# Optimization experiments

Measured on AMD Instinct MI355X. Metric: run time of the kernel, lower is better.

The kernel has to match this reference:

```python
import jax, jax.numpy as jnp
import numpy as np

V, B, T, C, H, L = 32000, 4, 1024, 1024, 16, 8
HS = C // H  # head_size = 64


def _ln(x, g, b):
    m = x.mean(-1, keepdims=True)
    v = x.var(-1, keepdims=True)
    return (x - m) / jnp.sqrt(v + 1e-5) * g + b


def setup_inputs() -> dict:
    key = jax.random.key(0)
    ks = jax.random.split(key, 24)
    s = 0.02
    inp = {
        "idx": jax.random.randint(ks[0], (B, T), 0, V, dtype=jnp.int64),
        "tok_emb": jax.random.normal(ks[1], (V, C), jnp.float32) * s,
        "pos_emb": jax.random.normal(ks[2], (T, C), jnp.float32) * s,
        "Wq": jax.random.normal(ks[3], (L, H, C, HS), jnp.float32) * s,
        "Wk": jax.random.normal(ks[4], (L, H, C, HS), jnp.float32) * s,
        "Wv": jax.random.normal(ks[5], (L, H, C, HS), jnp.float32) * s,
        "Ph_w": jax.random.normal(ks[6], (L, H, HS, C), jnp.float32) * s,
        "Ph_b": jnp.zeros((L, H, C), jnp.float32),
        "Pm_w": jax.random.normal(ks[7], (L, C, C), jnp.float32) * s,
        "Pm_b": jnp.zeros((L, C), jnp.float32),
        "ln1_g": jnp.ones((L, C), jnp.float32),
        "ln1_b": jnp.zeros((L, C), jnp.float32),
        "ln2_g": jnp.ones((L, C), jnp.float32),
        "ln2_b": jnp.zeros((L, C), jnp.float32),
        "W1": jax.random.normal(ks[8], (L, C, 4 * C), jnp.float32) * s,
        "b1": jnp.zeros((L, 4 * C), jnp.float32),
        "W2": jax.random.normal(ks[9], (L, 4 * C, C), jnp.float32) * s,
        "b2": jnp.zeros((L, C), jnp.float32),
        "lnf_g": jnp.ones((C,), jnp.float32),
        "lnf_b": jnp.zeros((C,), jnp.float32),
        "head_w": jax.random.normal(ks[10], (C, V), jnp.float32) * s,
        "head_b": jnp.zeros((V,), jnp.float32),
    }
    return inp


def reference(idx, tok_emb, pos_emb, Wq, Wk, Wv, Ph_w, Ph_b, Pm_w, Pm_b,
              ln1_g, ln1_b, ln2_g, ln2_b, W1, b1, W2, b2, lnf_g, lnf_b,
              head_w, head_b):
    Bx, Tx = idx.shape
    x = tok_emb[idx] + pos_emb[:Tx]  # [B,T,C]
    mask = jnp.tril(jnp.ones((Tx, Tx), bool))
    scale = x.shape[-1] ** -0.5  # NOTE: original scales by n_embd**-0.5, not head_size
    n_layers = Wq.shape[0]
    for l in range(n_layers):
        xn = _ln(x, ln1_g[l], ln1_b[l])
        q = jnp.einsum('btc,hcs->bhts', xn, Wq[l])
        k = jnp.einsum('btc,hcs->bhts', xn, Wk[l])
        v = jnp.einsum('btc,hcs->bhts', xn, Wv[l])
        wei = jnp.einsum('bhts,bhus->bhtu', q, k) * scale
        wei = jnp.where(mask, wei, -jnp.inf)
        wei = jax.nn.softmax(wei, axis=-1)
        o = jnp.einsum('bhtu,bhus->bhts', wei, v)  # [B,H,T,HS]
        per = jnp.einsum('bhts,hsc->bhtc', o, Ph_w[l]) + Ph_b[l][None, :, None, :]
        sa = per.sum(axis=1) @ Pm_w[l] + Pm_b[l]  # combine heads, final proj
        x = x + sa
        xn2 = _ln(x, ln2_g[l], ln2_b[l])
        h = jax.nn.gelu(xn2 @ W1[l] + b1[l], approximate=False)
        x = x + h @ W2[l] + b2[l]
    x = _ln(x, lnf_g, lnf_b)
    return x @ head_w + head_b  # logits [B,T,V]
```

## Files before the change

kernel.cpp:

```cpp
#include <hip/hip_runtime.h>
#include <hip/hip_bf16.h>
#include <math.h>

static constexpr int V = 32000, B = 4, T = 1024, C = 1024, H = 16, NL = 8, HS = 64;
static constexpr int M = B * T;

typedef __bf16 bf16x8 __attribute__((ext_vector_type(8)));
typedef __bf16 bf16x4 __attribute__((ext_vector_type(4)));
typedef float f32x4 __attribute__((ext_vector_type(4)));

#define AS1 __attribute__((address_space(1)))
#define AS3 __attribute__((address_space(3)))

__global__ void k_embed(const int* __restrict__ idx, const float* __restrict__ tok,
                        const float* __restrict__ pos, float* __restrict__ x) {
  int g = blockIdx.x * blockDim.x + threadIdx.x;
  if (g >= M * C / 4) return;
  int c4 = g & 255;
  int bt = g >> 8;
  int t = bt & (T - 1);
  int row = idx[bt];
  float4 tv = *(const float4*)(tok + (size_t)row * C + c4 * 4);
  float4 pv = *(const float4*)(pos + (size_t)t * C + c4 * 4);
  float4 o;
  o.x = tv.x + pv.x; o.y = tv.y + pv.y; o.z = tv.z + pv.z; o.w = tv.w + pv.w;
  *(float4*)(x + (size_t)bt * C + c4 * 4) = o;
}

__global__ __launch_bounds__(256) void k_ln_bf(const float* __restrict__ x, const float* __restrict__ g,
                                               const float* __restrict__ b, __hip_bfloat16* __restrict__ y) {
  int row = blockIdx.x, tid = threadIdx.x;
  float4 v = ((const float4*)(x + (size_t)row * C))[tid];
  float s = v.x + v.y + v.z + v.w;
  float ss = v.x * v.x + v.y * v.y + v.z * v.z + v.w * v.w;
  for (int off = 32; off > 0; off >>= 1) {
    s += __shfl_down(s, off);
    ss += __shfl_down(ss, off);
  }
  __shared__ float sb[4], qb[4];
  int wid = tid >> 6;
  if ((tid & 63) == 0) { sb[wid] = s; qb[wid] = ss; }
  __syncthreads();
  float st = sb[0] + sb[1] + sb[2] + sb[3];
  float qt = qb[0] + qb[1] + qb[2] + qb[3];
  float mean = st * (1.0f / C);
  float var = qt * (1.0f / C) - mean * mean;
  float rstd = rsqrtf(var + 1e-5f);
  float4 gv = ((const float4*)g)[tid];
  float4 bv = ((const float4*)b)[tid];
  union { __hip_bfloat16 h[4]; ushort4 u; } pk;
  pk.h[0] = __float2bfloat16((v.x - mean) * rstd * gv.x + bv.x);
  pk.h[1] = __float2bfloat16((v.y - mean) * rstd * gv.y + bv.y);
  pk.h[2] = __float2bfloat16((v.z - mean) * rstd * gv.z + bv.z);
  pk.h[3] = __float2bfloat16((v.w - mean) * rstd * gv.w + bv.w);
  *(ushort4*)(y + (size_t)row * C + tid * 4) = pk.u;
}

__global__ __launch_bounds__(256) void k_transp(const float* __restrict__ in, __hip_bfloat16* __restrict__ out,
                                                int K, int N) {
  __shared__ float t[64][65];
  int n0 = blockIdx.x * 64, k0 = blockIdx.y * 64;
  int tx = threadIdx.x & 15, ty = threadIdx.x >> 4;
#pragma unroll
  for (int i = 0; i < 64; i += 16) {
    float4 v = *(const float4*)(in + (size_t)(k0 + ty + i) * N + n0 + tx * 4);
    t[ty + i][tx * 4 + 0] = v.x;
    t[ty + i][tx * 4 + 1] = v.y;
    t[ty + i][tx * 4 + 2] = v.z;
    t[ty + i][tx * 4 + 3] = v.w;
  }
  __syncthreads();
#pragma unroll
  for (int i = 0; i < 64; i += 16) {
    int n = ty + i;
    union { __hip_bfloat16 h[4]; ushort4 u; } pk;
#pragma unroll
    for (int j = 0; j < 4; ++j) pk.h[j] = __float2bfloat16(t[tx * 4 + j][n]);
    *(ushort4*)(out + (size_t)(n0 + n) * K + k0 + tx * 4) = pk.u;
  }
}

__global__ void k_conv(const float* __restrict__ in, __hip_bfloat16* __restrict__ out, int n4) {
  int g = blockIdx.x * blockDim.x + threadIdx.x;
  if (g >= n4) return;
  float4 v = ((const float4*)in)[g];
  union { __hip_bfloat16 h[4]; ushort4 u; } pk;
  pk.h[0] = __float2bfloat16(v.x);
  pk.h[1] = __float2bfloat16(v.y);
  pk.h[2] = __float2bfloat16(v.z);
  pk.h[3] = __float2bfloat16(v.w);
  ((ushort4*)out)[g] = pk.u;
}

__global__ __launch_bounds__(256) void k_prep_qkv(const float* __restrict__ Wq, const float* __restrict__ Wk,
                                                  const float* __restrict__ Wv, __hip_bfloat16* __restrict__ out) {
  int z = blockIdx.y;
  int sel = z >> 4, h = z & 15;
  const float* W = sel == 0 ? Wq : (sel == 1 ? Wk : Wv);
  const float* in = W + (size_t)h * C * HS;
  __hip_bfloat16* o = out + ((size_t)sel * 1024 + h * 64) * C;
  __shared__ float t[64][65];
  int k0 = blockIdx.x * 64;
  int tx = threadIdx.x & 15, ty = threadIdx.x >> 4;
#pragma unroll
  for (int i = 0; i < 64; i += 16) {
    float4 v = *(const float4*)(in + (size_t)(k0 + ty + i) * HS + tx * 4);
    t[ty + i][tx * 4 + 0] = v.x;
    t[ty + i][tx * 4 + 1] = v.y;
    t[ty + i][tx * 4 + 2] = v.z;
    t[ty + i][tx * 4 + 3] = v.w;
  }
  __syncthreads();
#pragma unroll
  for (int i = 0; i < 64; i += 16) {
    int n = ty + i;
    union { __hip_bfloat16 h4[4]; ushort4 u; } pk;
#pragma unroll
    for (int j = 0; j < 4; ++j) pk.h4[j] = __float2bfloat16(t[tx * 4 + j][n]);
    *(ushort4*)(o + (size_t)n * C + k0 + tx * 4) = pk.u;
  }
}

__global__ void k_bsum(const float* __restrict__ phb, float* __restrict__ bs) {
  int c = blockIdx.x * blockDim.x + threadIdx.x;
  if (c < C) {
    float s = 0.0f;
    for (int h = 0; h < H; ++h) s += phb[(size_t)h * C + c];
    bs[c] = s;
  }
}

__global__ void k_biascomb(const float* __restrict__ bsum, const float* __restrict__ Pm,
                           const float* __restrict__ Pmb, float* __restrict__ bc) {
  int c = blockIdx.x * blockDim.x + threadIdx.x;
  if (c < C) {
    float s = Pmb[c];
    for (int j = 0; j < C; ++j) s += bsum[j] * Pm[(size_t)j * C + c];
    bc[c] = s;
  }
}

template <int BIAS, int GELU, int RES, int OUTBF>
__global__ __launch_bounds__(256) void k_gemm_bf(const __hip_bfloat16* __restrict__ A,
                                                 const __hip_bfloat16* __restrict__ Bt,
                                                 void* Cout, const float* __restrict__ bias,
                                                 const float* res, int N, int K) {
  __shared__ __align__(16) __hip_bfloat16 As[128 * 32];
  __shared__ __align__(16) __hip_bfloat16 Bs[128 * 32];
  int bm = blockIdx.y * 128, bn = blockIdx.x * 128;
  int tid = threadIdx.x;
  int w = tid >> 6, l = tid & 63;
  int wr = (w >> 1) * 64, wc = (w & 1) * 64;
  int lr = l >> 2;
  int lk = (l & 3) * 8;
  int fr = l & 15;
  int fk = (l >> 4) * 8;
  const __hip_bfloat16* Ag = A + (size_t)bm * K;
  const __hip_bfloat16* Bg = Bt + (size_t)bn * K;
  f32x4 acc[4][4];
#pragma unroll
  for (int m = 0; m < 4; ++m)
#pragma unroll
    for (int n = 0; n < 4; ++n) acc[m][n] = (f32x4){0.f, 0.f, 0.f, 0.f};

  for (int k0 = 0; k0 < K; k0 += 32) {
    __syncthreads();
#pragma unroll
    for (int i = 0; i < 2; ++i) {
      int seg = w * 2 + i;
      int r = seg * 16 + lr;
      __builtin_amdgcn_global_load_lds((const AS1 void*)(Ag + (size_t)r * K + k0 + lk),
                                       (AS3 void*)(As + seg * 512), 16, 0, 0);
      __builtin_amdgcn_global_load_lds((const AS1 void*)(Bg + (size_t)r * K + k0 + lk),
                                       (AS3 void*)(Bs + seg * 512), 16, 0, 0);
    }
    __syncthreads();
    bf16x8 af[4], bfr[4];
#pragma unroll
    for (int m = 0; m < 4; ++m) af[m] = *(const bf16x8*)(As + ((size_t)(wr + m * 16 + fr)) * 32 + fk);
#pragma unroll
    for (int n = 0; n < 4; ++n) bfr[n] = *(const bf16x8*)(Bs + ((size_t)(wc + n * 16 + fr)) * 32 + fk);
#pragma unroll
    for (int m = 0; m < 4; ++m)
#pragma unroll
      for (int n = 0; n < 4; ++n)
        acc[m][n] = __builtin_amdgcn_mfma_f32_16x16x32_bf16(af[m], bfr[n], acc[m][n], 0, 0, 0);
  }
  int crow0 = (l >> 4) * 4;
  int ccol = l & 15;
#pragma unroll
  for (int m = 0; m < 4; ++m) {
    int row = bm + wr + m * 16 + crow0;
#pragma unroll
    for (int n = 0; n < 4; ++n) {
      int col = bn + wc + n * 16 + ccol;
      float bv = BIAS ? bias[col] : 0.0f;
#pragma unroll
      for (int r = 0; r < 4; ++r) {
        float v = acc[m][n][r] + bv;
        if (GELU) v = 0.5f * v * (1.0f + erff(v * 0.70710678118f));
        if (RES) v += res[(size_t)(row + r) * N + col];
        if (OUTBF)
          ((__hip_bfloat16*)Cout)[(size_t)(row + r) * N + col] = __float2bfloat16(v);
        else
          ((float*)Cout)[(size_t)(row + r) * N + col] = v;
      }
    }
  }
}

template <int BIAS, int GELU, int RES, int OUTBF>
__global__ __launch_bounds__(512, 2) void k_gemm256(const __hip_bfloat16* __restrict__ Ah,
                                                    const __hip_bfloat16* __restrict__ Bth,
                                                    void* Cout, const float* __restrict__ bias,
                                                    const float* res, int N, int K) {
  __shared__ __align__(16) __bf16 As[2][256 * 64];
  __shared__ __align__(16) __bf16 Bs[2][256 * 64];
  const __bf16* A = (const __bf16*)Ah;
  const __bf16* Bt = (const __bf16*)Bth;
  const int nx = N >> 8;
  const int bid = blockIdx.x;
  const int sw = ((bid & 7) * ((int)gridDim.x >> 3)) + (bid >> 3);
  const int bn = (sw % nx) << 8;
  const int bm = (sw / nx) << 8;
  const int tid = threadIdx.x, w = tid >> 6, l = tid & 63;
  const int wm = w >> 2, wn = w & 3;
  const int fr = l & 15, fg = l >> 4;
  const int srow = w * 8 + (l >> 3);
  const int scolb = ((l & 7) << 4) ^ ((l & 8) << 3) ^ ((l & 16) << 1) ^ ((l & 32) >> 1);
  const __bf16* Ag = A + (size_t)(bm + srow) * K + (scolb >> 1);
  const __bf16* Bg = Bt + (size_t)(bn + srow) * K + (scolb >> 1);
  const int arow = wm * 128 + fr;
  const int brow = wn * 64 + fr;
  const int kswz = ((fr & 1) << 6) | ((fr & 2) << 4) | ((fr & 4) << 2);

  f32x4 acc[8][4];
#pragma unroll
  for (int m = 0; m < 8; ++m)
#pragma unroll
    for (int n = 0; n < 4; ++n) acc[m][n] = (f32x4){0.f, 0.f, 0.f, 0.f};

  auto stage = [&](int bufi, size_t kel) {
    const __bf16* ag_ = Ag + kel;
    const __bf16* bg_ = Bg + kel;
#pragma unroll
    for (int jj = 0; jj < 4; ++jj)
      __builtin_amdgcn_global_load_lds((const AS1 void*)(ag_ + (size_t)jj * 64 * K),
                                       (AS3 void*)(&As[bufi][jj * 4096 + w * 512]), 16, 0, 0);
#pragma unroll
    for (int jj = 0; jj < 4; ++jj)
      __builtin_amdgcn_global_load_lds((const AS1 void*)(bg_ + (size_t)jj * 64 * K),
                                       (AS3 void*)(&Bs[bufi][jj * 4096 + w * 512]), 16, 0, 0);
  };

  const int NT = K >> 6;
  stage(0, 0);
  asm volatile("s_waitcnt vmcnt(0)" ::: "memory");
  __builtin_amdgcn_sched_barrier(0);
  __builtin_amdgcn_s_barrier();
  __builtin_amdgcn_sched_barrier(0);

  for (int t = 0; t < NT; ++t) {
    const int cb = t & 1;
    const int nb = cb ^ 1;
    bf16x8 af[4][2], bv[4][2];

#define RD_A(MG, KS) \
  (*(const bf16x8*)(&As[cb][(arow + (MG) * 16) * 64 + ((((KS) * 64 + fg * 16) ^ kswz) >> 1)]))
#define RD_B(NG, KS) \
  (*(const bf16x8*)(&Bs[cb][(brow + (NG) * 16) * 64 + ((((KS) * 64 + fg * 16) ^ kswz) >> 1)]))
#define BAR() \
  __builtin_amdgcn_sched_barrier(0); __builtin_amdgcn_s_barrier(); __builtin_amdgcn_sched_barrier(0)

#pragma unroll
    for (int m = 0; m < 4; ++m) {
      af[m][0] = RD_A(m, 0);
      af[m][1] = RD_A(m, 1);
    }
#pragma unroll
    for (int n = 0; n < 2; ++n) {
      bv[n][0] = RD_B(n, 0);
      bv[n][1] = RD_B(n, 1);
    }
    if (t + 1 < NT) stage(nb, (size_t)(t + 1) * 64);
    BAR();
    __builtin_amdgcn_s_setprio(1);
#pragma unroll
    for (int m = 0; m < 4; ++m)
#pragma unroll
      for (int n = 0; n < 2; ++n)
#pragma unroll
        for (int ks = 0; ks < 2; ++ks)
          acc[m][n] = __builtin_amdgcn_mfma_f32_16x16x32_bf16(af[m][ks], bv[n][ks], acc[m][n], 0, 0, 0);
    __builtin_amdgcn_s_setprio(0);
    BAR();

#pragma unroll
    for (int n = 0; n < 2; ++n) {
      bv[2 + n][0] = RD_B(2 + n, 0);
      bv[2 + n][1] = RD_B(2 + n, 1);
    }
    BAR();
    __builtin_amdgcn_s_setprio(1);
#pragma unroll
    for (int m = 0; m < 4; ++m)
#pragma unroll
      for (int n = 0; n < 2; ++n)
#pragma unroll
        for (int ks = 0; ks < 2; ++ks)
          acc[m][2 + n] = __builtin_amdgcn_mfma_f32_16x16x32_bf16(af[m][ks], bv[2 + n][ks], acc[m][2 + n], 0, 0, 0);
    __builtin_amdgcn_s_setprio(0);
    BAR();

#pragma unroll
    for (int m = 0; m < 4; ++m) {
      af[m][0] = RD_A(4 + m, 0);
      af[m][1] = RD_A(4 + m, 1);
    }
    BAR();
    __builtin_amdgcn_s_setprio(1);
#pragma unroll
    for (int m = 0; m < 4; ++m)
#pragma unroll
      for (int n = 0; n < 4; ++n)
#pragma unroll
        for (int ks = 0; ks < 2; ++ks)
          acc[4 + m][n] = __builtin_amdgcn_mfma_f32_16x16x32_bf16(af[m][ks], bv[n][ks], acc[4 + m][n], 0, 0, 0);
    __builtin_amdgcn_s_setprio(0);
    asm volatile("s_waitcnt vmcnt(0)" ::: "memory");
    BAR();
#undef RD_A
#undef RD_B
#undef BAR
  }

#pragma unroll
  for (int mg = 0; mg < 8; ++mg) {
    int row = bm + wm * 128 + mg * 16 + fg * 4;
#pragma unroll
    for (int n = 0; n < 4; ++n) {
      int col = bn + wn * 64 + n * 16 + fr;
      float bvx = BIAS ? bias[col] : 0.0f;
#pragma unroll
      for (int r = 0; r < 4; ++r) {
        float v = acc[mg][n][r] + bvx;
        if (GELU) v = 0.5f * v * (1.0f + erff(v * 0.70710678118f));
        if (RES) v += res[(size_t)(row + r) * N + col];
        if (OUTBF)
          ((__hip_bfloat16*)Cout)[(size_t)(row + r) * N + col] = __float2bfloat16(v);
        else
          ((float*)Cout)[(size_t)(row + r) * N + col] = v;
      }
    }
  }
}

__global__ __launch_bounds__(256) void k_attn(const __hip_bfloat16* __restrict__ qkvh,
                                              __hip_bfloat16* __restrict__ o) {
  const __bf16* qkv = (const __bf16*)qkvh;
  int qi = blockIdx.x;
  int bh = blockIdx.y;
  int b = bh >> 4, h = bh & 15;
  int tid = threadIdx.x;
  int w = tid >> 6, l = tid & 63;
  int fr = l & 15, fg = l >> 4;
  int qw = qi * 64 + w * 16;

  __shared__ __align__(16) __bf16 Ks[32][72];
  __shared__ __align__(16) __bf16 Vs[32][76];
  __shared__ __align__(16) __bf16 Ps[4][16][40];

  const size_t bT = (size_t)b * T;
  bf16x8 a_q[2];
  {
    const __bf16* qp = qkv + (bT + qw + fr) * 3072 + h * 64 + fg * 8;
    a_q[0] = *(const bf16x8*)qp;
    a_q[1] = *(const bf16x8*)(qp + 32);
  }
  f32x4 acc_o[4];
#pragma unroll
  for (int n = 0; n < 4; ++n) acc_o[n] = (f32x4){0.f, 0.f, 0.f, 0.f};
  float mrow[4] = {-1e30f, -1e30f, -1e30f, -1e30f};
  float lrow[4] = {0.f, 0.f, 0.f, 0.f};

  int sr = tid >> 3;
  int sc = (tid & 7) * 8;
  int ntile = (qi + 1) * 2;
  for (int t = 0; t < ntile; ++t) {
    int kv0 = t * 32;
    __syncthreads();
    {
      const __bf16* kp = qkv + (bT + kv0 + sr) * 3072 + 1024 + h * 64 + sc;
      bf16x8 k8 = *(const bf16x8*)kp;
      bf16x8 v8 = *(const bf16x8*)(kp + 1024);
      *(bf16x8*)&Ks[sr][sc] = k8;
      *(bf16x4*)&Vs[sr][sc] = __builtin_shufflevector(v8, v8, 0, 1, 2, 3);
      *(bf16x4*)&Vs[sr][sc + 4] = __builtin_shufflevector(v8, v8, 4, 5, 6, 7);
    }
    __syncthreads();
    if (kv0 > qw + 15) continue;

    f32x4 s0 = (f32x4){0.f, 0.f, 0.f, 0.f}, s1 = s0;
    s0 = __builtin_amdgcn_mfma_f32_16x16x32_bf16(a_q[0], *(const bf16x8*)&Ks[fr][fg * 8], s0, 0, 0, 0);
    s0 = __builtin_amdgcn_mfma_f32_16x16x32_bf16(a_q[1], *(const bf16x8*)&Ks[fr][32 + fg * 8], s0, 0, 0, 0);
    s1 = __builtin_amdgcn_mfma_f32_16x16x32_bf16(a_q[0], *(const bf16x8*)&Ks[16 + fr][fg * 8], s1, 0, 0, 0);
    s1 = __builtin_amdgcn_mfma_f32_16x16x32_bf16(a_q[1], *(const bf16x8*)&Ks[16 + fr][32 + fg * 8], s1, 0, 0, 0);

    int qrow = qw + fg * 4;
#pragma unroll
    for (int r = 0; r < 4; ++r) { s0[r] *= 0.03125f; s1[r] *= 0.03125f; }
    if (kv0 + 31 > qw) {
#pragma unroll
      for (int r = 0; r < 4; ++r) {
        if (kv0 + fr > qrow + r) s0[r] = -1e30f;
        if (kv0 + 16 + fr > qrow + r) s1[r] = -1e30f;
      }
    }
    float tm[4], psum[4], alpha[4];
#pragma unroll
    for (int r = 0; r < 4; ++r) tm[r] = fmaxf(s0[r], s1[r]);
#pragma unroll
    for (int off = 1; off < 16; off <<= 1)
#pragma unroll
      for (int r = 0; r < 4; ++r) tm[r] = fmaxf(tm[r], __shfl_xor(tm[r], off));
#pragma unroll
    for (int r = 0; r < 4; ++r) {
      float mnew = fmaxf(mrow[r], tm[r]);
      alpha[r] = __expf(mrow[r] - mnew);
      mrow[r] = mnew;
      float p0 = __expf(s0[r] - mnew);
      float p1 = __expf(s1[r] - mnew);
      s0[r] = p0; s1[r] = p1;
      psum[r] = p0 + p1;
    }
#pragma unroll
    for (int off = 1; off < 16; off <<= 1)
#pragma unroll
      for (int r = 0; r < 4; ++r) psum[r] += __shfl_xor(psum[r], off);
#pragma unroll
    for (int r = 0; r < 4; ++r) lrow[r] = lrow[r] * alpha[r] + psum[r];
#pragma unroll
    for (int n = 0; n < 4; ++n)
#pragma unroll
      for (int r = 0; r < 4; ++r) acc_o[n][r] *= alpha[r];

#pragma unroll
    for (int r = 0; r < 4; ++r) {
      Ps[w][fg * 4 + r][fr] = (__bf16)s0[r];
      Ps[w][fg * 4 + r][16 + fr] = (__bf16)s1[r];
    }
    bf16x8 a_p = *(const bf16x8*)&Ps[w][fr][fg * 8];
#pragma unroll
    for (int n = 0; n < 4; ++n) {
      bf16x8 bvv;
#pragma unroll
      for (int j = 0; j < 8; ++j) bvv[j] = Vs[fg * 8 + j][n * 16 + fr];
      acc_o[n] = __builtin_amdgcn_mfma_f32_16x16x32_bf16(a_p, bvv, acc_o[n], 0, 0, 0);
    }
  }
  float inv[4];
#pragma unroll
  for (int r = 0; r < 4; ++r) inv[r] = 1.0f / lrow[r];
  __bf16* ob = (__bf16*)o;
#pragma unroll
  for (int n = 0; n < 4; ++n)
#pragma unroll
    for (int r = 0; r < 4; ++r)
      ob[(bT + qw + fg * 4 + r) * 1024 + h * 64 + n * 16 + fr] = (__bf16)(acc_o[n][r] * inv[r]);
}

extern "C" void kernel_launch(void* const* d_in, const int* in_sizes, int n_in,
                              void* d_out, int out_size, void* d_ws, size_t ws_size,
                              hipStream_t stream) {
  const int* idx = (const int*)d_in[0];
  const float* tok = (const float*)d_in[1];
  const float* pos = (const float*)d_in[2];
  const float* Wq = (const float*)d_in[3];
  const float* Wk = (const float*)d_in[4];
  const float* Wv = (const float*)d_in[5];
  const float* Phw = (const float*)d_in[6];
  const float* Phb = (const float*)d_in[7];
  const float* Pmw = (const float*)d_in[8];
  const float* Pmb = (const float*)d_in[9];
  const float* ln1g = (const float*)d_in[10];
  const float* ln1b = (const float*)d_in[11];
  const float* ln2g = (const float*)d_in[12];
  const float* ln2b = (const float*)d_in[13];
  const float* W1 = (const float*)d_in[14];
  const float* b1 = (const float*)d_in[15];
  const float* W2 = (const float*)d_in[16];
  const float* b2 = (const float*)d_in[17];
  const float* lnfg = (const float*)d_in[18];
  const float* lnfb = (const float*)d_in[19];
  const float* headw = (const float*)d_in[20];
  const float* headb = (const float*)d_in[21];
  float* out = (float*)d_out;

  char* p = (char*)d_ws;
  float* x = (float*)p;                       p += (size_t)M * C * 4;
  float* bsumv = (float*)p;                   p += 4096;
  float* bcv = (float*)p;                     p += 4096;
  char* layer_region = p;
  __hip_bfloat16* qkvb = (__hip_bfloat16*)p;  p += (size_t)M * 3072 * 2;
  __hip_bfloat16* ob = (__hip_bfloat16*)p;    p += (size_t)M * C * 2;
  __hip_bfloat16* hb = (__hip_bfloat16*)p;    p += (size_t)M * 4 * C * 2;
  __hip_bfloat16* wt = (__hip_bfloat16*)p;    p += (size_t)4 * C * C * 2;
  __hip_bfloat16* wtPmT = (__hip_bfloat16*)p; p += (size_t)C * C * 2;
  __hip_bfloat16* wtPh = (__hip_bfloat16*)p;  p += (size_t)C * C * 2;
  __hip_bfloat16* wcombT = (__hip_bfloat16*)p; p += (size_t)C * C * 2;
  __hip_bfloat16* xn = (__hip_bfloat16*)p;    p += (size_t)M * C * 2;
  __hip_bfloat16* wt_head = (__hip_bfloat16*)layer_region;

  k_embed<<<(M * C / 4 + 255) / 256, 256, 0, stream>>>(idx, tok, pos, x);

  for (int l = 0; l < NL; ++l) {
    k_ln_bf<<<M, 256, 0, stream>>>(x, ln1g + (size_t)l * C, ln1b + (size_t)l * C, xn);
    k_prep_qkv<<<dim3(16, 48), 256, 0, stream>>>(Wq + (size_t)l * H * C * HS, Wk + (size_t)l * H * C * HS,
                                                 Wv + (size_t)l * H * C * HS, wt);
    k_gemm256<0, 0, 0, 1><<<(3072 / 256) * (M / 256), 512, 0, stream>>>(xn, wt, qkvb, nullptr, nullptr, 3072, C);
    k_attn<<<dim3(T / 64, B * H), 256, 0, stream>>>(qkvb, ob);
    k_bsum<<<(C + 255) / 256, 256, 0, stream>>>(Phb + (size_t)l * H * C, bsumv);
    k_transp<<<dim3(16, 16), 256, 0, stream>>>(Pmw + (size_t)l * C * C, wtPmT, C, C);
    k_conv<<<(C * C / 4 + 255) / 256, 256, 0, stream>>>(Phw + (size_t)l * H * HS * C, wtPh, C * C / 4);
    k_gemm_bf<0, 0, 0, 1><<<dim3(C / 128, C / 128), 256, 0, stream>>>(wtPmT, wtPh, wcombT, nullptr, nullptr, C, C);
    k_biascomb<<<(C + 255) / 256, 256, 0, stream>>>(bsumv, Pmw + (size_t)l * C * C, Pmb + (size_t)l * C, bcv);
    k_gemm_bf<1, 0, 1, 0><<<dim3(C / 128, M / 128), 256, 0, stream>>>(ob, wcombT, x, bcv, x, C, C);
    k_ln_bf<<<M, 256, 0, stream>>>(x, ln2g + (size_t)l * C, ln2b + (size_t)l * C, xn);
    k_transp<<<dim3(64, 16), 256, 0, stream>>>(W1 + (size_t)l * C * 4 * C, wt, C, 4 * C);
    k_gemm256<1, 1, 0, 1><<<(4 * C / 256) * (M / 256), 512, 0, stream>>>(xn, wt, hb, b1 + (size_t)l * 4 * C, nullptr, 4 * C, C);
    k_transp<<<dim3(16, 64), 256, 0, stream>>>(W2 + (size_t)l * 4 * C * C, wt, 4 * C, C);
    k_gemm_bf<1, 0, 1, 0><<<dim3(C / 128, M / 128), 256, 0, stream>>>(hb, wt, x, b2 + (size_t)l * C, x, C, 4 * C);
  }

  k_ln_bf<<<M, 256, 0, stream>>>(x, lnfg, lnfb, xn);
  k_transp<<<dim3(500, 16), 256, 0, stream>>>(headw, wt_head, C, V);
  k_gemm256<1, 0, 0, 0><<<(V / 256) * (M / 256), 512, 0, stream>>>(xn, wt_head, out, headb, nullptr, V, C);
}
```

Baseline: 3.967 ms.

## Split 256x256 GEMM K-tile into two halves with finer-grained async staging

The 256-tile GEMM now stores each 64-wide K tile as two 32-wide halves in LDS with a new swizzle. The next tile's halves are issued one at a time, and partial vmcnt waits replace the full drain, so global-to-LDS loads overlap MFMA work more continuously and fewer barriers are needed per iteration. All 8x4 fragments are loaded per half, which raises register pressure. Separately, the bias-combine kernel splits the 1024-long reduction across four wavefronts with a shared-memory reduce, giving it more parallelism.

```diff
diff --git a/kernel.cpp b/kernel.cpp
--- a/kernel.cpp
+++ b/kernel.cpp
@@ -130,14 +130,16 @@
   }
 }
 
-__global__ void k_biascomb(const float* __restrict__ bsum, const float* __restrict__ Pm,
-                           const float* __restrict__ Pmb, float* __restrict__ bc) {
-  int c = blockIdx.x * blockDim.x + threadIdx.x;
-  if (c < C) {
-    float s = Pmb[c];
-    for (int j = 0; j < C; ++j) s += bsum[j] * Pm[(size_t)j * C + c];
-    bc[c] = s;
-  }
+__global__ __launch_bounds__(256) void k_biascomb(const float* __restrict__ bsum, const float* __restrict__ Pm,
+                                                  const float* __restrict__ Pmb, float* __restrict__ bc) {
+  int c = blockIdx.x * 64 + (threadIdx.x & 63);
+  int part = threadIdx.x >> 6;
+  float s = 0.0f;
+  for (int j = part * 256; j < part * 256 + 256; ++j) s += bsum[j] * Pm[(size_t)j * C + c];
+  __shared__ float red[4][64];
+  red[part][threadIdx.x & 63] = s;
+  __syncthreads();
+  if (threadIdx.x < 64) bc[c] = Pmb[c] + red[0][threadIdx.x] + red[1][threadIdx.x] + red[2][threadIdx.x] + red[3][threadIdx.x];
 }
 
 template <int BIAS, int GELU, int RES, int OUTBF>
@@ -214,8 +216,8 @@
                                                     const __hip_bfloat16* __restrict__ Bth,
                                                     void* Cout, const float* __restrict__ bias,
                                                     const float* res, int N, int K) {
-  __shared__ __align__(16) __bf16 As[2][256 * 64];
-  __shared__ __align__(16) __bf16 Bs[2][256 * 64];
+  __shared__ __align__(16) __bf16 As[2][2 * 8192];
+  __shared__ __align__(16) __bf16 Bs[2][2 * 8192];
   const __bf16* A = (const __bf16*)Ah;
   const __bf16* Bt = (const __bf16*)Bth;
   const int nx = N >> 8;
@@ -226,13 +228,13 @@
   const int tid = threadIdx.x, w = tid >> 6, l = tid & 63;
   const int wm = w >> 2, wn = w & 3;
   const int fr = l & 15, fg = l >> 4;
-  const int srow = w * 8 + (l >> 3);
-  const int scolb = ((l & 7) << 4) ^ ((l & 8) << 3) ^ ((l & 16) << 1) ^ ((l & 32) >> 1);
-  const __bf16* Ag = A + (size_t)(bm + srow) * K + (scolb >> 1);
-  const __bf16* Bg = Bt + (size_t)(bn + srow) * K + (scolb >> 1);
+  const int srow = w * 32 + (l >> 2);
+  const int scole = ((((l & 3) << 4) ^ ((l & 8) << 2) ^ (l & 16)) >> 1);
+  const __bf16* Ag = A + (size_t)(bm + srow) * K + scole;
+  const __bf16* Bg = Bt + (size_t)(bn + srow) * K + scole;
   const int arow = wm * 128 + fr;
   const int brow = wn * 64 + fr;
-  const int kswz = ((fr & 1) << 6) | ((fr & 2) << 4) | ((fr & 4) << 2);
+  const int kswz = ((fr & 2) << 4) | ((fr & 4) << 2);
 
   f32x4 acc[8][4];
 #pragma unroll
@@ -240,99 +242,68 @@
 #pragma unroll
     for (int n = 0; n < 4; ++n) acc[m][n] = (f32x4){0.f, 0.f, 0.f, 0.f};
 
-  auto stage = [&](int bufi, size_t kel) {
-    const __bf16* ag_ = Ag + kel;
-    const __bf16* bg_ = Bg + kel;
-#pragma unroll
-    for (int jj = 0; jj < 4; ++jj)
-      __builtin_amdgcn_global_load_lds((const AS1 void*)(ag_ + (size_t)jj * 64 * K),
-                                       (AS3 void*)(&As[bufi][jj * 4096 + w * 512]), 16, 0, 0);
-#pragma unroll
-    for (int jj = 0; jj < 4; ++jj)
-      __builtin_amdgcn_global_load_lds((const AS1 void*)(bg_ + (size_t)jj * 64 * K),
-                                       (AS3 void*)(&Bs[bufi][jj * 4096 + w * 512]), 16, 0, 0);
+  auto stage = [&](int bufi, int half, int t) {
+    size_t kb = (size_t)t * 64 + half * 32;
+#pragma unroll
+    for (int jj = 0; jj < 2; ++jj) {
+      __builtin_amdgcn_global_load_lds((const AS1 void*)(Ag + (size_t)jj * 16 * K + kb),
+                                       (AS3 void*)(&As[bufi][half * 8192 + (w * 32 + jj * 16) * 32]), 16, 0, 0);
+      __builtin_amdgcn_global_load_lds((const AS1 void*)(Bg + (size_t)jj * 16 * K + kb),
+                                       (AS3 void*)(&Bs[bufi][half * 8192 + (w * 32 + jj * 16) * 32]), 16, 0, 0);
+    }
   };
 
+#define RD_A(MG, HALF) \
+  (*(const bf16x8*)(&As[cb][(HALF) * 8192 + (arow + (MG) * 16) * 32 + (((fg * 16) ^ kswz) >> 1)]))
+#define RD_B(NG, HALF) \
+  (*(const bf16x8*)(&Bs[cb][(HALF) * 8192 + (brow + (NG) * 16) * 32 + (((fg * 16) ^ kswz) >> 1)]))
+
   const int NT = K >> 6;
-  stage(0, 0);
-  asm volatile("s_waitcnt vmcnt(0)" ::: "memory");
-  __builtin_amdgcn_sched_barrier(0);
-  __builtin_amdgcn_s_barrier();
-  __builtin_amdgcn_sched_barrier(0);
+  stage(0, 0, 0);
+  stage(0, 1, 0);
 
   for (int t = 0; t < NT; ++t) {
     const int cb = t & 1;
     const int nb = cb ^ 1;
-    bf16x8 af[4][2], bv[4][2];
-
-#define RD_A(MG, KS) \
-  (*(const bf16x8*)(&As[cb][(arow + (MG) * 16) * 64 + ((((KS) * 64 + fg * 16) ^ kswz) >> 1)]))
-#define RD_B(NG, KS) \
-  (*(const bf16x8*)(&Bs[cb][(brow + (NG) * 16) * 64 + ((((KS) * 64 + fg * 16) ^ kswz) >> 1)]))
-#define BAR() \
-  __builtin_amdgcn_sched_barrier(0); __builtin_amdgcn_s_barrier(); __builtin_amdgcn_sched_barrier(0)
-
-#pragma unroll
-    for (int m = 0; m < 4; ++m) {
-      af[m][0] = RD_A(m, 0);
-      af[m][1] = RD_A(m, 1);
-    }
-#pragma unroll
-    for (int n = 0; n < 2; ++n) {
-      bv[n][0] = RD_B(n, 0);
-      bv[n][1] = RD_B(n, 1);
-    }
-    if (t + 1 < NT) stage(nb, (size_t)(t + 1) * 64);
-    BAR();
+    bf16x8 af[8], bv[4];
+
+    asm volatile("s_waitcnt vmcnt(4)" ::: "memory");
+    __builtin_amdgcn_s_barrier();
+    __builtin_amdgcn_sched_barrier(0);
+#pragma unroll
+    for (int m = 0; m < 8; ++m) af[m] = RD_A(m, 0);
+#pragma unroll
+    for (int n = 0; n < 4; ++n) bv[n] = RD_B(n, 0);
+    if (t + 1 < NT) stage(nb, 0, t + 1);
     __builtin_amdgcn_s_setprio(1);
 #pragma unroll
-    for (int m = 0; m < 4; ++m)
-#pragma unroll
-      for (int n = 0; n < 2; ++n)
-#pragma unroll
-        for (int ks = 0; ks < 2; ++ks)
-          acc[m][n] = __builtin_amdgcn_mfma_f32_16x16x32_bf16(af[m][ks], bv[n][ks], acc[m][n], 0, 0, 0);
+    for (int m = 0; m < 8; ++m)
+#pragma unroll
+      for (int n = 0; n < 4; ++n)
+        acc[m][n] = __builtin_amdgcn_mfma_f32_16x16x32_bf16(af[m], bv[n], acc[m][n], 0, 0, 0);
     __builtin_amdgcn_s_setprio(0);
-    BAR();
-
-#pragma unroll
-    for (int n = 0; n < 2; ++n) {
-      bv[2 + n][0] = RD_B(2 + n, 0);
-      bv[2 + n][1] = RD_B(2 + n, 1);
-    }
-    BAR();
+
+    if (t + 1 < NT)
+      asm volatile("s_waitcnt vmcnt(4)" ::: "memory");
+    else
+      asm volatile("s_waitcnt vmcnt(0)" ::: "memory");
+    __builtin_amdgcn_s_barrier();
+    __builtin_amdgcn_sched_barrier(0);
+#pragma unroll
+    for (int m = 0; m < 8; ++m) af[m] = RD_A(m, 1);
+#pragma unroll
+    for (int n = 0; n < 4; ++n) bv[n] = RD_B(n, 1);
+    if (t + 1 < NT) stage(nb, 1, t + 1);
     __builtin_amdgcn_s_setprio(1);
 #pragma unroll
-    for (int m = 0; m < 4; ++m)
-#pragma unroll
-      for (int n = 0; n < 2; ++n)
-#pragma unroll
-        for (int ks = 0; ks < 2; ++ks)
-          acc[m][2 + n] = __builtin_amdgcn_mfma_f32_16x16x32_bf16(af[m][ks], bv[2 + n][ks], acc[m][2 + n], 0, 0, 0);
+    for (int m = 0; m < 8; ++m)
+#pragma unroll
+      for (int n = 0; n < 4; ++n)
+        acc[m][n] = __builtin_amdgcn_mfma_f32_16x16x32_bf16(af[m], bv[n], acc[m][n], 0, 0, 0);
     __builtin_amdgcn_s_setprio(0);
-    BAR();
-
-#pragma unroll
-    for (int m = 0; m < 4; ++m) {
-      af[m][0] = RD_A(4 + m, 0);
-      af[m][1] = RD_A(4 + m, 1);
-    }
-    BAR();
-    __builtin_amdgcn_s_setprio(1);
-#pragma unroll
-    for (int m = 0; m < 4; ++m)
-#pragma unroll
-      for (int n = 0; n < 4; ++n)
-#pragma unroll
-        for (int ks = 0; ks < 2; ++ks)
-          acc[4 + m][n] = __builtin_amdgcn_mfma_f32_16x16x32_bf16(af[m][ks], bv[n][ks], acc[4 + m][n], 0, 0, 0);
-    __builtin_amdgcn_s_setprio(0);
-    asm volatile("s_waitcnt vmcnt(0)" ::: "memory");
-    BAR();
+  }
 #undef RD_A
 #undef RD_B
-#undef BAR
-  }
 
 #pragma unroll
   for (int mg = 0; mg < 8; ++mg) {
@@ -523,7 +494,7 @@
     k_transp<<<dim3(16, 16), 256, 0, stream>>>(Pmw + (size_t)l * C * C, wtPmT, C, C);
     k_conv<<<(C * C / 4 + 255) / 256, 256, 0, stream>>>(Phw + (size_t)l * H * HS * C, wtPh, C * C / 4);
     k_gemm_bf<0, 0, 0, 1><<<dim3(C / 128, C / 128), 256, 0, stream>>>(wtPmT, wtPh, wcombT, nullptr, nullptr, C, C);
-    k_biascomb<<<(C + 255) / 256, 256, 0, stream>>>(bsumv, Pmw + (size_t)l * C * C, Pmb + (size_t)l * C, bcv);
+    k_biascomb<<<16, 256, 0, stream>>>(bsumv, Pmw + (size_t)l * C * C, Pmb + (size_t)l * C, bcv);
     k_gemm_bf<1, 0, 1, 0><<<dim3(C / 128, M / 128), 256, 0, stream>>>(ob, wcombT, x, bcv, x, C, C);
     k_ln_bf<<<M, 256, 0, stream>>>(x, ln2g + (size_t)l * C, ln2b + (size_t)l * C, xn);
     k_transp<<<dim3(64, 16), 256, 0, stream>>>(W1 + (size_t)l * C * 4 * C, wt, C, 4 * C);
```

Measured after the change: 3.601 ms. 1.1x faster.
